# Kernel optimization log

Measured on AMD Instinct MI355X. Metric: run time of the kernel, lower is better.

Reference implementation:

```python
import jax, jax.numpy as jnp
import numpy as np

C = 128
HEADS = 4
GROUPS = 8
SHAPE = (1, C, 8, 24, 32)  # N, C, D, H, W
EPS = 1e-5


def setup_inputs() -> dict:
    key = jax.random.key(0)
    ks = jax.random.split(key, 3)
    x = jax.random.normal(ks[0], SHAPE, dtype=jnp.float32)
    mask = jnp.ones((1, 1) + SHAPE[2:], dtype=jnp.float32)
    qkv_w = jax.random.normal(ks[1], (3 * C, C), dtype=jnp.float32) * (1.0 / np.sqrt(C))
    qkv_b = jnp.zeros((3 * C,), dtype=jnp.float32)
    proj_w = jax.random.normal(ks[2], (C, C), dtype=jnp.float32) * (1.0 / np.sqrt(C))
    proj_b = jnp.zeros((C,), dtype=jnp.float32)
    return {
        'x': x, 'mask': mask,
        'gn_w': jnp.ones((C,), dtype=jnp.float32),
        'gn_b': jnp.zeros((C,), dtype=jnp.float32),
        'qkv_w': qkv_w, 'qkv_b': qkv_b,
        'proj_w': proj_w, 'proj_b': proj_b,
    }


def group_norm(x, w, b):
    N, Ch, D, H, W = x.shape
    xg = x.reshape(N, GROUPS, Ch // GROUPS, D, H, W)
    mu = jnp.mean(xg, axis=(2, 3, 4, 5), keepdims=True)
    var = jnp.var(xg, axis=(2, 3, 4, 5), keepdims=True)
    xg = (xg - mu) * jax.lax.rsqrt(var + EPS)
    x = xg.reshape(N, Ch, D, H, W)
    return x * w[None, :, None, None, None] + b[None, :, None, None, None]


def reference(x, mask, gn_w, gn_b, qkv_w, qkv_b, proj_w, proj_b):
    N, Ch, D, H, W = x.shape
    S = D * H * W
    hd = Ch // HEADS  # head dim
    xn = group_norm(x, gn_w, gn_b)
    # 1x1x1 conv == channel GEMM: [N,3C,S]
    qkv = jnp.einsum('ncs,oc->nos', xn.reshape(N, Ch, S), qkv_w) + qkv_b[None, :, None]
    q, k, v = jnp.split(qkv, 3, axis=1)
    # '(h c) s -> h s c' (head-major channel split)
    def to_heads(t):
        return t.reshape(N, HEADS, hd, S).transpose(0, 1, 3, 2)  # n h s c
    q, k, v = to_heads(q), to_heads(k), to_heads(v)
    scale = hd ** -0.5
    scores = jnp.einsum('nhic,nhjc->nhij', q, k) * scale
    probs = jax.nn.softmax(scores, axis=-1)
    out = jnp.einsum('nhij,nhjc->nhic', probs, v)
    # n h s c -> n (h c) s
    out = out.transpose(0, 1, 3, 2).reshape(N, Ch, S)
    out = jnp.einsum('ncs,oc->nos', out, proj_w) + proj_b[None, :, None]
    out = out.reshape(N, Ch, D, H, W)
    return (x + out) * mask, mask
```

## Files before the change

### kernel.cpp

```cpp
#include <hip/hip_runtime.h>
#include <hip/hip_bf16.h>
#include <cstddef>

typedef __bf16 bf16;
typedef __bf16 bf16x4 __attribute__((ext_vector_type(4)));
typedef __bf16 bf16x8 __attribute__((ext_vector_type(8)));
typedef float  f32x4  __attribute__((ext_vector_type(4)));

#define NC   128
#define NS   6144
#define HD   32
#define BKV  64
#define NSPLIT 4
#define NCH  ((NS / NSPLIT) / BKV)
#define GELEMS (16 * NS)
#define QK_SCALE (0.17677669529663689f * 1.4426950408889634f)

__device__ __forceinline__ f32x4 mfma16(bf16x8 a, bf16x8 b, f32x4 c) {
  return __builtin_amdgcn_mfma_f32_16x16x32_bf16(a, b, c, 0, 0, 0);
}
__device__ __forceinline__ void gl16(const bf16* g, void* s) {
  __builtin_amdgcn_global_load_lds((const __attribute__((address_space(1))) void*)g,
                                   (__attribute__((address_space(3))) void*)s, 16, 0, 0);
}
__device__ __forceinline__ int swz(int b) { return b ^ (((b >> 7) & 7) << 4); }
__device__ __forceinline__ unsigned cvtpk(float lo, float hi) {
  unsigned r;
  asm("v_cvt_pk_bf16_f32 %0, %1, %2" : "=v"(r) : "v"(lo), "v"(hi));
  return r;
}
__device__ __forceinline__ bf16x8 mkfrag(unsigned a, unsigned b, unsigned c, unsigned d) {
  union { unsigned u[4]; bf16x8 v; } t;
  t.u[0] = a; t.u[1] = b; t.u[2] = c; t.u[3] = d;
  return t.v;
}
__device__ __forceinline__ int vperm(int s6) {
  return ((s6 & 12) << 2) | (((s6 >> 4) & 3) << 2) | (s6 & 3);
}

__global__ __launch_bounds__(256) void k_prep_stats(
    const float* __restrict__ qkv_w, const float* __restrict__ qkv_b,
    const float* __restrict__ proj_w, const float* __restrict__ x,
    bf16* __restrict__ wq, bf16* __restrict__ wp, float* __restrict__ bias_s,
    float* __restrict__ partials) {
  int bid = blockIdx.x;
  int tid = threadIdx.x;
  if (bid < 192) {
    int i = bid * 256 + tid;
    if (i < 3 * NC * NC) {
      float v = qkv_w[i];
      if (i < NC * NC) v *= QK_SCALE;
      wq[i] = (bf16)v;
    }
    if (i < NC * NC) wp[i] = (bf16)proj_w[i];
    if (i < 3 * NC) bias_s[i] = qkv_b[i] * ((i < NC) ? QK_SCALE : 1.0f);
    return;
  }
  int b = bid - 192;
  int g = b / 12, chunk = b % 12;
  float sum = 0.f, sq = 0.f;
  #pragma unroll
  for (int k = 0; k < 8; ++k) {
    int f4 = tid + k * 256;
    int c  = f4 >> 7;
    int s4 = f4 & 127;
    const float4 v = ((const float4*)x)[(size_t)(g * 16 + c) * (NS / 4) + chunk * 128 + s4];
    sum += v.x + v.y + v.z + v.w;
    sq  += v.x * v.x + v.y * v.y + v.z * v.z + v.w * v.w;
  }
  #pragma unroll
  for (int off = 32; off; off >>= 1) {
    sum += __shfl_down(sum, off, 64);
    sq  += __shfl_down(sq,  off, 64);
  }
  __shared__ float red[2][4];
  if ((tid & 63) == 0) { red[0][tid >> 6] = sum; red[1][tid >> 6] = sq; }
  __syncthreads();
  if (tid == 0) {
    partials[b * 2 + 0] = red[0][0] + red[0][1] + red[0][2] + red[0][3];
    partials[b * 2 + 1] = red[1][0] + red[1][1] + red[1][2] + red[1][3];
  }
}

__global__ __launch_bounds__(256) void k_qkv(
    const float* __restrict__ x, const float* __restrict__ partials,
    const float* __restrict__ gn_w, const float* __restrict__ gn_b,
    const bf16* __restrict__ wq, const float* __restrict__ bias_s,
    bf16* __restrict__ qg, bf16* __restrict__ kg, bf16* __restrict__ vtg) {
  int ot = blockIdx.x;
  int st = blockIdx.y;
  int tid = threadIdx.x;
  __shared__ __align__(16) char xn[64 * 256];
  __shared__ float swc[NC], sbc[NC];

  if (tid < NC) {
    int g = tid >> 4;
    float sum = 0.f, sq = 0.f;
    #pragma unroll
    for (int i = 0; i < 12; ++i) {
      sum += partials[(g * 12 + i) * 2 + 0];
      sq  += partials[(g * 12 + i) * 2 + 1];
    }
    float mean = sum * (1.0f / GELEMS);
    float var  = sq  * (1.0f / GELEMS) - mean * mean;
    float rstd = rsqrtf(var + 1e-5f);
    float wc = gn_w[tid] * rstd;
    swc[tid] = wc;
    sbc[tid] = gn_b[tid] - mean * wc;
  }
  __syncthreads();

  int s_local = tid & 63;
  int s_glob  = st * 64 + s_local;
  int wk = tid >> 6;
  #pragma unroll
  for (int i = 0; i < 4; ++i) {
    int c0 = (wk * 4 + i) * 8;
    bf16x8 ov;
    #pragma unroll
    for (int j = 0; j < 8; ++j) {
      int c = c0 + j;
      ov[j] = (bf16)(x[(size_t)c * NS + s_glob] * swc[c] + sbc[c]);
    }
    *(bf16x8*)(xn + ((s_local * 256 + c0 * 2) ^ ((s_local & 7) << 4))) = ov;
  }
  __syncthreads();

  int w = tid >> 6, l = tid & 63;
  int lr = l & 15, lg = l >> 4;
  int o_base = ot * 64 + (w >> 1) * 32;
  int sl_base = (w & 1) * 32;
  f32x4 acc[2][2] = {};
  #pragma unroll
  for (int k0 = 0; k0 < NC; k0 += 32) {
    bf16x8 a[2], b[2];
    #pragma unroll
    for (int m = 0; m < 2; ++m)
      a[m] = *(const bf16x8*)(wq + (size_t)(o_base + m * 16 + lr) * NC + k0 + lg * 8);
    #pragma unroll
    for (int n = 0; n < 2; ++n) {
      int row = sl_base + n * 16 + lr;
      b[n] = *(const bf16x8*)(xn + ((row * 256 + (k0 + lg * 8) * 2) ^ ((row & 7) << 4)));
    }
    #pragma unroll
    for (int m = 0; m < 2; ++m)
      #pragma unroll
      for (int n = 0; n < 2; ++n)
        acc[m][n] = mfma16(a[m], b[n], acc[m][n]);
  }

  __syncthreads();
  bf16* ot_lds = (bf16*)xn;
  const bool is_v = (ot >= 4);
  #pragma unroll
  for (int m = 0; m < 2; ++m)
    #pragma unroll
    for (int n = 0; n < 2; ++n)
      #pragma unroll
      for (int r = 0; r < 4; ++r) {
        int o_l = (w >> 1) * 32 + m * 16 + lg * 4 + r;
        int s_l = (w & 1) * 32 + n * 16 + lr;
        int o = ot * 64 + o_l;
        bf16 v = (bf16)(acc[m][n][r] + bias_s[o]);
        if (is_v) ot_lds[o_l * 72 + vperm(s_l)] = v;
        else      ot_lds[s_l * 72 + o_l]        = v;
      }
  __syncthreads();

  if (!is_v) {
    bf16* dst = (ot < 2) ? qg : kg;
    int head0 = (ot & 1) * 2;
    int c8 = tid & 3, s_l = tid >> 2;
    size_t s = (size_t)st * 64 + s_l;
    #pragma unroll
    for (int i = 0; i < 2; ++i) {
      bf16x8 v = *(const bf16x8*)(ot_lds + s_l * 72 + i * 32 + c8 * 8);
      *(bf16x8*)(dst + ((size_t)(head0 + i) * NS + s) * HD + c8 * 8) = v;
    }
  } else {
    int head0 = (ot - 4) * 2;
    int c_l = tid >> 2;
    int head = head0 + (c_l >> 5), c32 = c_l & 31;
    bf16* drow = vtg + ((size_t)head * HD + c32) * NS + st * 64;
    #pragma unroll
    for (int i = 0; i < 2; ++i) {
      int pos8 = (tid & 3) * 2 + i;
      bf16x8 v = *(const bf16x8*)(ot_lds + c_l * 72 + pos8 * 8);
      *(bf16x8*)(drow + pos8 * 8) = v;
    }
  }
}

__global__ __launch_bounds__(256, 6) void k_attn(
    const bf16* __restrict__ qg, const bf16* __restrict__ kg, const bf16* __restrict__ vtg,
    bf16* __restrict__ accP, float* __restrict__ ml) {
  const int h = blockIdx.y, sp = blockIdx.z;
  const int tid = threadIdx.x;
  const int w = tid >> 6, l = tid & 63;
  const int lr = l & 15, lg = l >> 4;
  const int qrow0 = blockIdx.x * 64 + w * 16;

  __shared__ __align__(16) char kbuf[2][4096];
  __shared__ __align__(16) char vbuf[2][4096];
  const int kswz  = ((lr >> 1) & 7) << 4;
  const int vswz  = (lr & 7) << 4;

  const bf16* qp = qg + (size_t)h * NS * HD;
  const bf16* kp = kg + (size_t)h * NS * HD;
  const bf16* vp = vtg + (size_t)h * HD * NS;

  bf16x8 qf = *(const bf16x8*)(qp + (size_t)(qrow0 + lr) * HD + lg * 8);

  bf16x8 ones;
  #pragma unroll
  for (int j = 0; j < 8; ++j) ones[j] = (bf16)1.0f;

  f32x4 acc0 = {}, acc1 = {};
  f32x4 lacc = {};
  const f32x4 zed = {};
  const int kv_beg = sp * (NS / NSPLIT);

  const int o_st = w * 1024 + (l << 4);
  const int u_st = swz(o_st);
  const bf16* ksrc = kp + (size_t)(kv_beg + (u_st >> 6)) * HD + ((u_st & 63) >> 1);
  const bf16* vsrc = vp + (size_t)(u_st >> 7) * NS + kv_beg + ((u_st & 127) >> 1);

  f32x4 sv[4];
  bf16x8 pf0, pf1;

  auto packP = [&]() {
    float e0[4], e1[4], e2[4], e3[4];
    #pragma unroll
    for (int r = 0; r < 4; ++r) {
      e0[r] = __builtin_amdgcn_exp2f(sv[0][r]);
      e1[r] = __builtin_amdgcn_exp2f(sv[1][r]);
      e2[r] = __builtin_amdgcn_exp2f(sv[2][r]);
      e3[r] = __builtin_amdgcn_exp2f(sv[3][r]);
    }
    pf0 = mkfrag(cvtpk(e0[0], e0[1]), cvtpk(e0[2], e0[3]),
                 cvtpk(e1[0], e1[1]), cvtpk(e1[2], e1[3]));
    pf1 = mkfrag(cvtpk(e2[0], e2[1]), cvtpk(e2[2], e2[3]),
                 cvtpk(e3[0], e3[1]), cvtpk(e3[2], e3[3]));
  };
  auto vfrag = [&](const char* vb, int row, int kk) -> bf16x8 {
    int base = (row + lr) * 128 + lg * 32 + kk * 16;
    return *(const bf16x8*)(vb + (base ^ vswz));
  };

  gl16(ksrc, kbuf[0] + w * 1024);
  gl16(vsrc, vbuf[0] + w * 1024);
  gl16(ksrc + BKV * HD, kbuf[1] + w * 1024);
  __syncthreads();
  #pragma unroll
  for (int t4 = 0; t4 < 4; ++t4) {
    bf16x8 kf = *(const bf16x8*)(kbuf[0] + (((t4 * 16 + lr) * 64 + lg * 16) ^ kswz));
    sv[t4] = mfma16(kf, qf, zed);
  }
  packP();

  for (int t = 0; t < NCH; ++t) {
    const int cur = t & 1, nxt = cur ^ 1;
    const bool hn = (t + 1 < NCH);
    __syncthreads();
    if (hn) gl16(vsrc + (size_t)(t + 1) * BKV, vbuf[nxt] + w * 1024);
    if (t + 2 < NCH) gl16(ksrc + (size_t)(t + 2) * BKV * HD, kbuf[cur] + w * 1024);
    if (hn) {
      #pragma unroll
      for (int t4 = 0; t4 < 4; ++t4) {
        bf16x8 kf = *(const bf16x8*)(kbuf[nxt] + (((t4 * 16 + lr) * 64 + lg * 16) ^ kswz));
        sv[t4] = mfma16(kf, qf, zed);
      }
    }
    {
      const char* vb = vbuf[cur];
      acc0 = mfma16(vfrag(vb, 0,  0), pf0, acc0);
      acc1 = mfma16(vfrag(vb, 16, 0), pf0, acc1);
      lacc = mfma16(ones, pf0, lacc);
      acc0 = mfma16(vfrag(vb, 0,  1), pf1, acc0);
      acc1 = mfma16(vfrag(vb, 16, 1), pf1, acc1);
      lacc = mfma16(ones, pf1, lacc);
    }
    if (hn) packP();
  }

  bf16* base = accP + (size_t)(h * NSPLIT + sp) * 8 * NS * 4;
  size_t qrow = qrow0 + lr;
  bf16x4 o0, o1;
  #pragma unroll
  for (int r = 0; r < 4; ++r) { o0[r] = (bf16)acc0[r]; o1[r] = (bf16)acc1[r]; }
  *(bf16x4*)(base + ((size_t)lg * NS + qrow) * 4)       = o0;
  *(bf16x4*)(base + ((size_t)(4 + lg) * NS + qrow) * 4) = o1;
  if (lg == 0)
    ml[(size_t)(h * NSPLIT + sp) * NS + qrow] = lacc[0];
}

__global__ __launch_bounds__(256) void k_proj(
    const bf16* __restrict__ wp, const bf16* __restrict__ accP, const float* __restrict__ ml,
    const float* __restrict__ proj_b, const float* __restrict__ x,
    const float* __restrict__ mask, float* __restrict__ out) {
  int ot = blockIdx.x;
  int st = blockIdx.y;
  int tid = threadIdx.x;
  __shared__ __align__(16) char at[32 * 256];

  int s_local = tid >> 3;
  int s = st * 32 + s_local;
  if (ot == 0 && tid < 32)
    out[(size_t)NC * NS + st * 32 + tid] = mask[st * 32 + tid];
  #pragma unroll
  for (int i = 0; i < 2; ++i) {
    int c0 = ((tid & 7) * 2 + i) * 8;
    int h = c0 >> 5;
    float L = 0.f;
    #pragma unroll
    for (int spl = 0; spl < NSPLIT; ++spl)
      L += ml[(size_t)(h * NSPLIT + spl) * NS + s];
    float inv = 1.0f / L;
    float o[8] = {};
    int cg0 = (c0 & 31) >> 2;
    #pragma unroll
    for (int spl = 0; spl < NSPLIT; ++spl) {
      const bf16* bp = accP + ((size_t)((h * NSPLIT + spl) * 8 + cg0) * NS + s) * 4;
      bf16x4 a0 = *(const bf16x4*)(bp);
      bf16x4 a1 = *(const bf16x4*)(bp + (size_t)NS * 4);
      #pragma unroll
      for (int j = 0; j < 4; ++j) {
        o[j]     += (float)a0[j];
        o[4 + j] += (float)a1[j];
      }
    }
    bf16x8 ov;
    #pragma unroll
    for (int j = 0; j < 8; ++j) ov[j] = (bf16)(o[j] * inv);
    *(bf16x8*)(at + ((s_local * 256 + c0 * 2) ^ ((s_local & 7) << 4))) = ov;
  }
  __syncthreads();

  int w = tid >> 6, l = tid & 63;
  int lr = l & 15, lg = l >> 4;
  int o_base = ot * 64 + (w >> 1) * 32;
  int sl_base = (w & 1) * 16;
  f32x4 acc[2] = {};
  #pragma unroll
  for (int k0 = 0; k0 < NC; k0 += 32) {
    bf16x8 a[2], b;
    #pragma unroll
    for (int m = 0; m < 2; ++m)
      a[m] = *(const bf16x8*)(wp + (size_t)(o_base + m * 16 + lr) * NC + k0 + lg * 8);
    {
      int row = sl_base + lr;
      b = *(const bf16x8*)(at + ((row * 256 + (k0 + lg * 8) * 2) ^ ((row & 7) << 4)));
    }
    #pragma unroll
    for (int m = 0; m < 2; ++m)
      acc[m] = mfma16(a[m], b, acc[m]);
  }
  #pragma unroll
  for (int m = 0; m < 2; ++m)
    #pragma unroll
    for (int r = 0; r < 4; ++r) {
      int o = o_base + m * 16 + lg * 4 + r;
      int sg = st * 32 + sl_base + lr;
      float v = acc[m][r] + proj_b[o] + x[(size_t)o * NS + sg];
      out[(size_t)o * NS + sg] = v * mask[sg];
    }
}

extern "C" void kernel_launch(void* const* d_in, const int* in_sizes, int n_in,
                              void* d_out, int out_size, void* d_ws, size_t ws_size,
                              hipStream_t stream) {
  const float* x      = (const float*)d_in[0];
  const float* mask   = (const float*)d_in[1];
  const float* gn_w   = (const float*)d_in[2];
  const float* gn_b   = (const float*)d_in[3];
  const float* qkv_w  = (const float*)d_in[4];
  const float* qkv_b  = (const float*)d_in[5];
  const float* proj_w = (const float*)d_in[6];
  const float* proj_b = (const float*)d_in[7];

  char* ws = (char*)d_ws;
  float* partials = (float*)(ws + 0);
  float* bias_s   = (float*)(ws + 1024);
  bf16*  wq       = (bf16*)(ws + 4096);
  bf16*  wp       = (bf16*)(ws + 102400);
  bf16*  qg       = (bf16*)(ws + 135168);
  bf16*  kg       = (bf16*)(ws + 1708032);
  bf16*  vtg      = (bf16*)(ws + 3280896);
  bf16*  accP     = (bf16*)(ws + 4853760);
  float* ml       = (float*)(ws + 11145216);
  float* out      = (float*)d_out;

  k_prep_stats<<<288, 256, 0, stream>>>(qkv_w, qkv_b, proj_w, x, wq, wp, bias_s, partials);
  k_qkv       <<<dim3(6, 96), 256, 0, stream>>>(x, partials, gn_w, gn_b, wq, bias_s, qg, kg, vtg);
  k_attn      <<<dim3(96, 4, NSPLIT), 256, 0, stream>>>(qg, kg, vtg, accP, ml);
  k_proj      <<<dim3(2, 192), 256, 0, stream>>>(wp, accP, ml, proj_b, x, mask, out);
}
```

Before: 56.76 us.

## Switch attention kernel to 32x32x16 MFMA with 32 query rows per wave

Rewrites the attention inner loop to use 32x32x16 bf16 MFMA tiles, with each wave handling 32 query rows instead of 16. The grid is halved and the K/V tiles are reused across twice as many queries. The softmax row sum is now accumulated in scalar adds plus a cross-half shuffle, replacing the extra MFMA against a ones vector. The V-transpose permutation helper changes to match the new fragment layout. This raises register pressure (launch bounds drop to 4 waves/SIMD) and halves the block count, which may reduce occupancy and latency hiding.

```diff
diff --git a/kernel.cpp b/kernel.cpp
--- a/kernel.cpp
+++ b/kernel.cpp
@@ -6,6 +6,7 @@
 typedef __bf16 bf16x4 __attribute__((ext_vector_type(4)));
 typedef __bf16 bf16x8 __attribute__((ext_vector_type(8)));
 typedef float  f32x4  __attribute__((ext_vector_type(4)));
+typedef float  f32x16 __attribute__((ext_vector_type(16)));
 
 #define NC   128
 #define NS   6144
@@ -19,6 +20,9 @@
 __device__ __forceinline__ f32x4 mfma16(bf16x8 a, bf16x8 b, f32x4 c) {
   return __builtin_amdgcn_mfma_f32_16x16x32_bf16(a, b, c, 0, 0, 0);
 }
+__device__ __forceinline__ f32x16 mfma32(bf16x8 a, bf16x8 b, f32x16 c) {
+  return __builtin_amdgcn_mfma_f32_32x32x16_bf16(a, b, c, 0, 0, 0);
+}
 __device__ __forceinline__ void gl16(const bf16* g, void* s) {
   __builtin_amdgcn_global_load_lds((const __attribute__((address_space(1))) void*)g,
                                    (__attribute__((address_space(3))) void*)s, 16, 0, 0);
@@ -34,8 +38,8 @@
   t.u[0] = a; t.u[1] = b; t.u[2] = c; t.u[3] = d;
   return t.v;
 }
-__device__ __forceinline__ int vperm(int s6) {
-  return ((s6 & 12) << 2) | (((s6 >> 4) & 3) << 2) | (s6 & 3);
+__device__ __forceinline__ int vperm(int k) {
+  return (((k >> 2) & 1) << 5) | (((k >> 4) & 3) << 3) | (((k >> 3) & 1) << 2) | (k & 3);
 }
 
 __global__ __launch_bounds__(256) void k_prep_stats(
@@ -191,33 +195,32 @@
   }
 }
 
-__global__ __launch_bounds__(256, 6) void k_attn(
+__global__ __launch_bounds__(256, 4) void k_attn(
     const bf16* __restrict__ qg, const bf16* __restrict__ kg, const bf16* __restrict__ vtg,
     bf16* __restrict__ accP, float* __restrict__ ml) {
   const int h = blockIdx.y, sp = blockIdx.z;
   const int tid = threadIdx.x;
   const int w = tid >> 6, l = tid & 63;
-  const int lr = l & 15, lg = l >> 4;
-  const int qrow0 = blockIdx.x * 64 + w * 16;
+  const int l31 = l & 31, hi = l >> 5;
+  const int qrow0 = blockIdx.x * 128 + w * 32;
 
   __shared__ __align__(16) char kbuf[2][4096];
   __shared__ __align__(16) char vbuf[2][4096];
-  const int kswz  = ((lr >> 1) & 7) << 4;
-  const int vswz  = (lr & 7) << 4;
+  const int kswz = ((l31 >> 1) & 7) << 4;
+  const int vswz = (l31 & 7) << 4;
+  const int ka0  = (l31 * 64 + hi * 16) ^ kswz;
+  const int ka1  = (l31 * 64 + 32 + hi * 16) ^ kswz;
 
   const bf16* qp = qg + (size_t)h * NS * HD;
   const bf16* kp = kg + (size_t)h * NS * HD;
   const bf16* vp = vtg + (size_t)h * HD * NS;
 
-  bf16x8 qf = *(const bf16x8*)(qp + (size_t)(qrow0 + lr) * HD + lg * 8);
-
-  bf16x8 ones;
-  #pragma unroll
-  for (int j = 0; j < 8; ++j) ones[j] = (bf16)1.0f;
-
-  f32x4 acc0 = {}, acc1 = {};
-  f32x4 lacc = {};
-  const f32x4 zed = {};
+  bf16x8 qf0 = *(const bf16x8*)(qp + (size_t)(qrow0 + l31) * HD + hi * 8);
+  bf16x8 qf1 = *(const bf16x8*)(qp + (size_t)(qrow0 + l31) * HD + 16 + hi * 8);
+
+  f32x16 Ot = {};
+  float l_r = 0.f;
+  const f32x16 zed16 = {};
   const int kv_beg = sp * (NS / NSPLIT);
 
   const int o_st = w * 1024 + (l << 4);
@@ -225,38 +228,37 @@
   const bf16* ksrc = kp + (size_t)(kv_beg + (u_st >> 6)) * HD + ((u_st & 63) >> 1);
   const bf16* vsrc = vp + (size_t)(u_st >> 7) * NS + kv_beg + ((u_st & 127) >> 1);
 
-  f32x4 sv[4];
-  bf16x8 pf0, pf1;
-
-  auto packP = [&]() {
-    float e0[4], e1[4], e2[4], e3[4];
-    #pragma unroll
-    for (int r = 0; r < 4; ++r) {
-      e0[r] = __builtin_amdgcn_exp2f(sv[0][r]);
-      e1[r] = __builtin_amdgcn_exp2f(sv[1][r]);
-      e2[r] = __builtin_amdgcn_exp2f(sv[2][r]);
-      e3[r] = __builtin_amdgcn_exp2f(sv[3][r]);
-    }
-    pf0 = mkfrag(cvtpk(e0[0], e0[1]), cvtpk(e0[2], e0[3]),
-                 cvtpk(e1[0], e1[1]), cvtpk(e1[2], e1[3]));
-    pf1 = mkfrag(cvtpk(e2[0], e2[1]), cvtpk(e2[2], e2[3]),
-                 cvtpk(e3[0], e3[1]), cvtpk(e3[2], e3[3]));
+  f32x16 sv0, sv1;
+  bf16x8 pf0, pf1, pf2, pf3;
+
+  auto packP = [&](f32x16& sv, bf16x8& fA, bf16x8& fB) {
+    float e[16];
+    #pragma unroll
+    for (int r = 0; r < 16; ++r) e[r] = __builtin_amdgcn_exp2f(sv[r]);
+    l_r += (((e[0] + e[1]) + (e[2] + e[3])) + ((e[4] + e[5]) + (e[6] + e[7])))
+         + (((e[8] + e[9]) + (e[10] + e[11])) + ((e[12] + e[13]) + (e[14] + e[15])));
+    fA = mkfrag(cvtpk(e[0], e[1]),  cvtpk(e[2], e[3]),
+                cvtpk(e[4], e[5]),  cvtpk(e[6], e[7]));
+    fB = mkfrag(cvtpk(e[8], e[9]),  cvtpk(e[10], e[11]),
+                cvtpk(e[12], e[13]), cvtpk(e[14], e[15]));
   };
-  auto vfrag = [&](const char* vb, int row, int kk) -> bf16x8 {
-    int base = (row + lr) * 128 + lg * 32 + kk * 16;
-    return *(const bf16x8*)(vb + (base ^ vswz));
+  auto vfrag = [&](const char* vb, int m) -> bf16x8 {
+    return *(const bf16x8*)(vb + ((l31 * 128 + hi * 64 + m * 16) ^ vswz));
+  };
+  auto qk = [&](const char* kb) {
+    sv0 = mfma32(*(const bf16x8*)(kb + ka0), qf0, zed16);
+    sv0 = mfma32(*(const bf16x8*)(kb + ka1), qf1, sv0);
+    sv1 = mfma32(*(const bf16x8*)(kb + ka0 + 2048), qf0, zed16);
+    sv1 = mfma32(*(const bf16x8*)(kb + ka1 + 2048), qf1, sv1);
   };
 
   gl16(ksrc, kbuf[0] + w * 1024);
   gl16(vsrc, vbuf[0] + w * 1024);
   gl16(ksrc + BKV * HD, kbuf[1] + w * 1024);
   __syncthreads();
-  #pragma unroll
-  for (int t4 = 0; t4 < 4; ++t4) {
-    bf16x8 kf = *(const bf16x8*)(kbuf[0] + (((t4 * 16 + lr) * 64 + lg * 16) ^ kswz));
-    sv[t4] = mfma16(kf, qf, zed);
-  }
-  packP();
+  qk(kbuf[0]);
+  packP(sv0, pf0, pf1);
+  packP(sv1, pf2, pf3);
 
   for (int t = 0; t < NCH; ++t) {
     const int cur = t & 1, nxt = cur ^ 1;
@@ -264,34 +266,33 @@
     __syncthreads();
     if (hn) gl16(vsrc + (size_t)(t + 1) * BKV, vbuf[nxt] + w * 1024);
     if (t + 2 < NCH) gl16(ksrc + (size_t)(t + 2) * BKV * HD, kbuf[cur] + w * 1024);
-    if (hn) {
-      #pragma unroll
-      for (int t4 = 0; t4 < 4; ++t4) {
-        bf16x8 kf = *(const bf16x8*)(kbuf[nxt] + (((t4 * 16 + lr) * 64 + lg * 16) ^ kswz));
-        sv[t4] = mfma16(kf, qf, zed);
-      }
-    }
+    if (hn) qk(kbuf[nxt]);
     {
       const char* vb = vbuf[cur];
-      acc0 = mfma16(vfrag(vb, 0,  0), pf0, acc0);
-      acc1 = mfma16(vfrag(vb, 16, 0), pf0, acc1);
-      lacc = mfma16(ones, pf0, lacc);
-      acc0 = mfma16(vfrag(vb, 0,  1), pf1, acc0);
-      acc1 = mfma16(vfrag(vb, 16, 1), pf1, acc1);
-      lacc = mfma16(ones, pf1, lacc);
-    }
-    if (hn) packP();
-  }
+      Ot = mfma32(vfrag(vb, 0), pf0, Ot);
+      Ot = mfma32(vfrag(vb, 1), pf1, Ot);
+      Ot = mfma32(vfrag(vb, 2), pf2, Ot);
+      Ot = mfma32(vfrag(vb, 3), pf3, Ot);
+    }
+    if (hn) {
+      packP(sv0, pf0, pf1);
+      packP(sv1, pf2, pf3);
+    }
+  }
+
+  l_r += __shfl_xor(l_r, 32, 64);
 
   bf16* base = accP + (size_t)(h * NSPLIT + sp) * 8 * NS * 4;
-  size_t qrow = qrow0 + lr;
-  bf16x4 o0, o1;
-  #pragma unroll
-  for (int r = 0; r < 4; ++r) { o0[r] = (bf16)acc0[r]; o1[r] = (bf16)acc1[r]; }
-  *(bf16x4*)(base + ((size_t)lg * NS + qrow) * 4)       = o0;
-  *(bf16x4*)(base + ((size_t)(4 + lg) * NS + qrow) * 4) = o1;
-  if (lg == 0)
-    ml[(size_t)(h * NSPLIT + sp) * NS + qrow] = lacc[0];
+  size_t qrow = qrow0 + l31;
+  #pragma unroll
+  for (int m = 0; m < 4; ++m) {
+    bf16x4 ov;
+    #pragma unroll
+    for (int j = 0; j < 4; ++j) ov[j] = (bf16)Ot[4 * m + j];
+    *(bf16x4*)(base + ((size_t)(hi + 2 * m) * NS + qrow) * 4) = ov;
+  }
+  if (hi == 0)
+    ml[(size_t)(h * NSPLIT + sp) * NS + qrow] = l_r;
 }
 
 __global__ __launch_bounds__(256) void k_proj(
@@ -392,6 +393,6 @@
 
   k_prep_stats<<<288, 256, 0, stream>>>(qkv_w, qkv_b, proj_w, x, wq, wp, bias_s, partials);
   k_qkv       <<<dim3(6, 96), 256, 0, stream>>>(x, partials, gn_w, gn_b, wq, bias_s, qg, kg, vtg);
-  k_attn      <<<dim3(96, 4, NSPLIT), 256, 0, stream>>>(qg, kg, vtg, accP, ml);
+  k_attn      <<<dim3(48, 4, NSPLIT), 256, 0, stream>>>(qg, kg, vtg, accP, ml);
   k_proj      <<<dim3(2, 192), 256, 0, stream>>>(wp, accP, ml, proj_b, x, mask, out);
 }
```

New measurement: 54.33 us, median of 2. -4.3%, faster.
